# Performance work log

Measured on AMD Instinct MI355X. Metric: run time of the kernel, lower is better.

Reference implementation:

```python
import jax, jax.numpy as jnp
import numpy as np

N = 100000   # nodes
E = 1600000  # edges (avg degree 16)
D = 128      # input feature dim
H = 128      # Config.hidden_dim
G = 64       # graphs in batch
OUT = 2      # output classes


def setup_inputs() -> dict:
    key = jax.random.key(0)
    ks = jax.random.split(key, 12)
    s = 0.05
    return {
        "x": jax.random.normal(ks[0], (N, D), dtype=jnp.float32),
        "edge_index": jax.random.randint(ks[1], (2, E), 0, N),
        "batch": jnp.sort(jax.random.randint(ks[2], (N,), 0, G)),
        "W1": jax.random.normal(ks[3], (H, D), dtype=jnp.float32) * s,
        "b1": jnp.zeros((H,), jnp.float32),
        "W2": jax.random.normal(ks[4], (H, H), dtype=jnp.float32) * s,
        "b2": jnp.zeros((H,), jnp.float32),
        "Wf1": jax.random.normal(ks[5], (H, H), dtype=jnp.float32) * s,
        "bf1": jnp.zeros((H,), jnp.float32),
        "Wf2": jax.random.normal(ks[6], (OUT, H), dtype=jnp.float32) * s,
        "bf2": jnp.zeros((OUT,), jnp.float32),
    }


def _gnn_layer(x, src, dst, W, b):
    # message(x_j) = Linear(x[src]); linear commutes with gather, so transform
    # node features once (N rows) instead of per-edge (E rows): same math.
    xw = x @ W.T + b                                   # [N, H]
    msg = xw[src]                                      # [E, H] gather
    summed = jax.ops.segment_sum(msg, dst, num_segments=N)            # [N, H]
    cnt = jax.ops.segment_sum(jnp.ones((src.shape[0],), x.dtype), dst,
                              num_segments=N)                          # [N]
    return summed / jnp.maximum(cnt, 1.0)[:, None]     # scatter-mean (0 for deg-0)


def reference(x, edge_index, batch, W1, b1, W2, b2, Wf1, bf1, Wf2, bf2):
    src, dst = edge_index[0], edge_index[1]
    h = jax.nn.relu(_gnn_layer(x, src, dst, W1, b1))
    h = jax.nn.relu(_gnn_layer(h, src, dst, W2, b2))
    g = jax.ops.segment_max(h, batch, num_segments=G)  # global_max_pool [G, H]
    z = jax.nn.relu(g @ Wf1.T + bf1)                   # fc (dropout = identity, eval)
    z = z @ Wf2.T + bf2                                # [G, OUT]
    return jax.nn.log_softmax(z, axis=1)
```

## Files before the change

### kernel.cpp

```cpp
#include <hip/hip_runtime.h>
#include <hip/hip_fp16.h>
#include <math.h>


#define SPLIT 64
#define BUCKET_SHIFT 8
#define BUCKET_SIZE 256
#define MAXBUCK 512
#define BIN_CHUNK 4096
#define CAP 4608
#define LSTR 136

typedef _Float16 half8 __attribute__((ext_vector_type(8)));
typedef _Float16 half4v __attribute__((ext_vector_type(4)));
typedef _Float16 half2v __attribute__((ext_vector_type(2)));
typedef float floatx4 __attribute__((ext_vector_type(4)));
typedef float floatx2 __attribute__((ext_vector_type(2)));

#define RFL(v) __builtin_amdgcn_readfirstlane(v)

__global__ void k_init(int* __restrict__ bcur, int* __restrict__ gstart,
                       int* __restrict__ gend,
                       const float* __restrict__ W1, const float* __restrict__ W2,
                       _Float16* __restrict__ w1h, _Float16* __restrict__ w2h,
                       int G, int nbuck) {
    int i = blockIdx.x * blockDim.x + threadIdx.x;
    if (i < nbuck) bcur[i] = i * CAP;
    if (i < G) { gstart[i] = 0; gend[i] = 0; }
    w1h[i] = (_Float16)W1[i];
    w2h[i] = (_Float16)W2[i];
}

__global__ __launch_bounds__(256) void k_bin(
        const int* __restrict__ src, const int* __restrict__ dst,
        int* __restrict__ bcur, int* __restrict__ staging,
        const int* __restrict__ batch, int* __restrict__ gstart,
        int* __restrict__ gend, int E, int N, int nbuck) {
    __shared__ int lh[MAXBUCK];
    __shared__ int lbase[MAXBUCK];
    __shared__ int lc[MAXBUCK];
    int t = threadIdx.x;
    for (int i = t; i < nbuck; i += 256) { lh[i] = 0; lc[i] = 0; }

    int n = blockIdx.x * 256 + t;
    if (n < N) {
        int b = batch[n];
        if (n == 0 || batch[n - 1] != b) gstart[b] = n;
        if (n == N - 1 || batch[n + 1] != b) gend[b] = n + 1;
    }
    __syncthreads();

    int base = blockIdx.x * BIN_CHUNK;
    if (base + BIN_CHUNK <= E) {
        int ds[16], ss[16];
        const int4* dv = (const int4*)(dst + base);
        const int4* sv = (const int4*)(src + base);
        #pragma unroll
        for (int j = 0; j < 4; ++j) {
            int4 d = dv[j * 256 + t];
            int4 s = sv[j * 256 + t];
            ds[j * 4 + 0] = d.x; ds[j * 4 + 1] = d.y;
            ds[j * 4 + 2] = d.z; ds[j * 4 + 3] = d.w;
            ss[j * 4 + 0] = s.x; ss[j * 4 + 1] = s.y;
            ss[j * 4 + 2] = s.z; ss[j * 4 + 3] = s.w;
        }
        #pragma unroll
        for (int q = 0; q < 16; ++q)
            atomicAdd(&lh[ds[q] >> BUCKET_SHIFT], 1);
        __syncthreads();
        for (int i = t; i < nbuck; i += 256)
            if (lh[i]) lbase[i] = atomicAdd(&bcur[i], lh[i]);
        __syncthreads();
        #pragma unroll
        for (int q = 0; q < 16; ++q) {
            int d = ds[q];
            int b = d >> BUCKET_SHIFT;
            int pos = lbase[b] + atomicAdd(&lc[b], 1);
            if (pos < (b + 1) * CAP)
                staging[pos] = ss[q] | ((d & (BUCKET_SIZE - 1)) << 24);
        }
    } else {
        for (int e = base + t; e < E; e += 256)
            atomicAdd(&lh[dst[e] >> BUCKET_SHIFT], 1);
        __syncthreads();
        for (int i = t; i < nbuck; i += 256)
            if (lh[i]) lbase[i] = atomicAdd(&bcur[i], lh[i]);
        __syncthreads();
        for (int e = base + t; e < E; e += 256) {
            int d = dst[e];
            int b = d >> BUCKET_SHIFT;
            int pos = lbase[b] + atomicAdd(&lc[b], 1);
            if (pos < (b + 1) * CAP)
                staging[pos] = src[e] | ((d & (BUCKET_SIZE - 1)) << 24);
        }
    }
}

__global__ __launch_bounds__(BUCKET_SIZE) void k_bcsr(
        const int* __restrict__ staging, const int* __restrict__ bcur,
        int* __restrict__ esrc, int* __restrict__ rowstart,
        int* __restrict__ deg, int N) {
    __shared__ int sw[CAP];
    __shared__ int lh[BUCKET_SIZE];
    __shared__ int lcur[BUCKET_SIZE];
    __shared__ int wsum[4];
    int b = blockIdx.x;
    int s = b * CAP;
    int e = min(bcur[b], s + CAP);
    int len = e - s;
    int t = threadIdx.x;
    lh[t] = 0;
    __syncthreads();
    for (int i = t; i < len; i += BUCKET_SIZE) {
        int p = staging[s + i];
        sw[i] = p;
        atomicAdd(&lh[((unsigned)p) >> 24], 1);
    }
    __syncthreads();
    int v = lh[t];
    int lane = t & 63;
    int wv = t >> 6;
    int inc = v;
    #pragma unroll
    for (int off = 1; off < 64; off <<= 1) {
        int x = __shfl_up(inc, off, 64);
        if (lane >= off) inc += x;
    }
    if (lane == 63) wsum[wv] = inc;
    __syncthreads();
    int woff = 0;
    #pragma unroll
    for (int k = 0; k < 3; ++k)
        if (k < wv) woff += wsum[k];
    int excl = woff + inc - v;
    int node = b * BUCKET_SIZE + t;
    if (node < N) { rowstart[node] = s + excl; deg[node] = v; }
    lcur[t] = excl;
    __syncthreads();
    for (int i = t; i < len; i += BUCKET_SIZE) {
        int p = sw[i];
        int local = ((unsigned)p) >> 24;
        int pos = atomicAdd(&lcur[local], 1);
        esrc[s + pos] = p & 0xFFFFFF;
    }
}

__device__ __forceinline__ void mfma_tile(const _Float16* sX,
                                          const _Float16* __restrict__ Wh,
                                          const float* __restrict__ bias,
                                          unsigned char* __restrict__ out8,
                                          int n0, int N, int t) {
    int w = t >> 6;
    int lane = t & 63;
    int quad = lane >> 4;
    int lrow = lane & 15;

    floatx4 acc[8];
    #pragma unroll
    for (int i = 0; i < 8; ++i) acc[i] = {0.f, 0.f, 0.f, 0.f};

    int arow = (w * 16 + lrow) * LSTR + quad * 8;
    #pragma unroll
    for (int k0 = 0; k0 < 128; k0 += 32) {
        half8 a = *(const half8*)&sX[arow + k0];
        #pragma unroll
        for (int ht = 0; ht < 8; ++ht) {
            half8 b = *(const half8*)(Wh + (ht * 16 + lrow) * 128 + quad * 8 + k0);
            acc[ht] = __builtin_amdgcn_mfma_f32_16x16x32_f16(a, b, acc[ht], 0, 0, 0);
        }
    }

    #pragma unroll
    for (int ht = 0; ht < 8; ++ht) {
        int h = ht * 16 + lrow;
        float bv = bias[h];
        #pragma unroll
        for (int r = 0; r < 4; ++r) {
            int node = n0 + w * 16 + quad * 4 + r;
            if (node < N) {
                float v = acc[ht][r] + bv;
                int pk = __builtin_amdgcn_cvt_pk_fp8_f32(v, v, 0, false);
                out8[(size_t)node * 128 + h] = (unsigned char)(pk & 0xFF);
            }
        }
    }
}

__global__ __launch_bounds__(512, 6) void k_gemm(const float* __restrict__ in,
                                                 const _Float16* __restrict__ Wh,
                                                 const float* __restrict__ bias,
                                                 unsigned char* __restrict__ out8,
                                                 int N) {
    __shared__ _Float16 sX[128 * LSTR];
    int t = threadIdx.x;
    int n0 = blockIdx.x * 128;

    #pragma unroll
    for (int it = 0; it < 8; ++it) {
        int lin = it * 512 + t;
        int r = lin >> 5;
        int c = (lin & 31) * 4;
        half4v xh = {0, 0, 0, 0};
        int n = n0 + r;
        if (n < N) {
            float4 xv = *(const float4*)(in + (size_t)n * 128 + c);
            xh = half4v{ (_Float16)xv.x, (_Float16)xv.y, (_Float16)xv.z, (_Float16)xv.w };
        }
        *(half4v*)&sX[r * LSTR + c] = xh;
    }
    __syncthreads();
    mfma_tile(sX, Wh, bias, out8, n0, N, t);
}

__global__ __launch_bounds__(512, 6) void k_ag(const unsigned char* __restrict__ in8,
                                               const int* __restrict__ esrc,
                                               const int* __restrict__ rowstart,
                                               const int* __restrict__ deg,
                                               const _Float16* __restrict__ Wh,
                                               const float* __restrict__ bias,
                                               unsigned char* __restrict__ out8,
                                               int N) {
    __shared__ _Float16 sX[128 * LSTR];
    int t = threadIdx.x;
    int w = t >> 6;
    int lane = t & 63;
    int n0 = blockIdx.x * 128;
    const unsigned short* in16 = (const unsigned short*)in8;

    for (int k = 0; k < 16; ++k) {
        int node = n0 + w * 16 + k;
        float sx = 0.f, sy = 0.f;
        int dd = 0;
        if (node < N) {
            int start = RFL(rowstart[node]);
            int d     = RFL(deg[node]);
            dd = d;
            floatx2 a0 = {0.f, 0.f}, a1 = {0.f, 0.f}, a2 = {0.f, 0.f}, a3 = {0.f, 0.f};
            int i = 0;
            for (; i + 8 <= d; i += 8) {
                int x0 = RFL(esrc[start + i + 0]);
                int x1 = RFL(esrc[start + i + 1]);
                int x2 = RFL(esrc[start + i + 2]);
                int x3 = RFL(esrc[start + i + 3]);
                int x4 = RFL(esrc[start + i + 4]);
                int x5 = RFL(esrc[start + i + 5]);
                int x6 = RFL(esrc[start + i + 6]);
                int x7 = RFL(esrc[start + i + 7]);
                unsigned u0 = in16[((size_t)x0 << 6) + lane];
                unsigned u1 = in16[((size_t)x1 << 6) + lane];
                unsigned u2 = in16[((size_t)x2 << 6) + lane];
                unsigned u3 = in16[((size_t)x3 << 6) + lane];
                unsigned u4 = in16[((size_t)x4 << 6) + lane];
                unsigned u5 = in16[((size_t)x5 << 6) + lane];
                unsigned u6 = in16[((size_t)x6 << 6) + lane];
                unsigned u7 = in16[((size_t)x7 << 6) + lane];
                floatx2 f0 = __builtin_amdgcn_cvt_pk_f32_fp8(u0, false);
                floatx2 f1 = __builtin_amdgcn_cvt_pk_f32_fp8(u1, false);
                floatx2 f2 = __builtin_amdgcn_cvt_pk_f32_fp8(u2, false);
                floatx2 f3 = __builtin_amdgcn_cvt_pk_f32_fp8(u3, false);
                floatx2 f4 = __builtin_amdgcn_cvt_pk_f32_fp8(u4, false);
                floatx2 f5 = __builtin_amdgcn_cvt_pk_f32_fp8(u5, false);
                floatx2 f6 = __builtin_amdgcn_cvt_pk_f32_fp8(u6, false);
                floatx2 f7 = __builtin_amdgcn_cvt_pk_f32_fp8(u7, false);
                a0.x += f0.x; a0.y += f0.y;  a1.x += f1.x; a1.y += f1.y;
                a2.x += f2.x; a2.y += f2.y;  a3.x += f3.x; a3.y += f3.y;
                a0.x += f4.x; a0.y += f4.y;  a1.x += f5.x; a1.y += f5.y;
                a2.x += f6.x; a2.y += f6.y;  a3.x += f7.x; a3.y += f7.y;
            }
            for (; i + 4 <= d; i += 4) {
                int x0 = RFL(esrc[start + i + 0]);
                int x1 = RFL(esrc[start + i + 1]);
                int x2 = RFL(esrc[start + i + 2]);
                int x3 = RFL(esrc[start + i + 3]);
                unsigned u0 = in16[((size_t)x0 << 6) + lane];
                unsigned u1 = in16[((size_t)x1 << 6) + lane];
                unsigned u2 = in16[((size_t)x2 << 6) + lane];
                unsigned u3 = in16[((size_t)x3 << 6) + lane];
                floatx2 f0 = __builtin_amdgcn_cvt_pk_f32_fp8(u0, false);
                floatx2 f1 = __builtin_amdgcn_cvt_pk_f32_fp8(u1, false);
                floatx2 f2 = __builtin_amdgcn_cvt_pk_f32_fp8(u2, false);
                floatx2 f3 = __builtin_amdgcn_cvt_pk_f32_fp8(u3, false);
                a0.x += f0.x; a0.y += f0.y;  a1.x += f1.x; a1.y += f1.y;
                a2.x += f2.x; a2.y += f2.y;  a3.x += f3.x; a3.y += f3.y;
            }
            for (; i < d; ++i) {
                int x0 = RFL(esrc[start + i]);
                unsigned u0 = in16[((size_t)x0 << 6) + lane];
                floatx2 f0 = __builtin_amdgcn_cvt_pk_f32_fp8(u0, false);
                a0.x += f0.x; a0.y += f0.y;
            }
            sx = (a0.x + a1.x) + (a2.x + a3.x);
            sy = (a0.y + a1.y) + (a2.y + a3.y);
        }
        float dm = fmaxf((float)dd, 1.0f);
        half2v hv = { (_Float16)fmaxf(sx / dm, 0.f),
                      (_Float16)fmaxf(sy / dm, 0.f) };
        *(half2v*)&sX[(w * 16 + k) * LSTR + lane * 2] = hv;
    }
    __syncthreads();
    mfma_tile(sX, Wh, bias, out8, n0, N, t);
}

__global__ __launch_bounds__(256) void k_agg(const unsigned char* __restrict__ in8,
                                             const int* __restrict__ esrc,
                                             const int* __restrict__ rowstart,
                                             const int* __restrict__ deg,
                                             _Float16* __restrict__ outh, int N) {
    int lane = threadIdx.x & 63;
    int node = blockIdx.x * 4 + (threadIdx.x >> 6);
    if (node >= N) return;
    int start = RFL(rowstart[node]);
    int d     = RFL(deg[node]);
    const unsigned short* in16 = (const unsigned short*)in8;

    floatx2 a0 = {0.f, 0.f}, a1 = {0.f, 0.f}, a2 = {0.f, 0.f}, a3 = {0.f, 0.f};

    int i = 0;
    for (; i + 8 <= d; i += 8) {
        int x0 = RFL(esrc[start + i + 0]);
        int x1 = RFL(esrc[start + i + 1]);
        int x2 = RFL(esrc[start + i + 2]);
        int x3 = RFL(esrc[start + i + 3]);
        int x4 = RFL(esrc[start + i + 4]);
        int x5 = RFL(esrc[start + i + 5]);
        int x6 = RFL(esrc[start + i + 6]);
        int x7 = RFL(esrc[start + i + 7]);
        unsigned u0 = in16[((size_t)x0 << 6) + lane];
        unsigned u1 = in16[((size_t)x1 << 6) + lane];
        unsigned u2 = in16[((size_t)x2 << 6) + lane];
        unsigned u3 = in16[((size_t)x3 << 6) + lane];
        unsigned u4 = in16[((size_t)x4 << 6) + lane];
        unsigned u5 = in16[((size_t)x5 << 6) + lane];
        unsigned u6 = in16[((size_t)x6 << 6) + lane];
        unsigned u7 = in16[((size_t)x7 << 6) + lane];
        floatx2 f0 = __builtin_amdgcn_cvt_pk_f32_fp8(u0, false);
        floatx2 f1 = __builtin_amdgcn_cvt_pk_f32_fp8(u1, false);
        floatx2 f2 = __builtin_amdgcn_cvt_pk_f32_fp8(u2, false);
        floatx2 f3 = __builtin_amdgcn_cvt_pk_f32_fp8(u3, false);
        floatx2 f4 = __builtin_amdgcn_cvt_pk_f32_fp8(u4, false);
        floatx2 f5 = __builtin_amdgcn_cvt_pk_f32_fp8(u5, false);
        floatx2 f6 = __builtin_amdgcn_cvt_pk_f32_fp8(u6, false);
        floatx2 f7 = __builtin_amdgcn_cvt_pk_f32_fp8(u7, false);
        a0.x += f0.x; a0.y += f0.y;  a1.x += f1.x; a1.y += f1.y;
        a2.x += f2.x; a2.y += f2.y;  a3.x += f3.x; a3.y += f3.y;
        a0.x += f4.x; a0.y += f4.y;  a1.x += f5.x; a1.y += f5.y;
        a2.x += f6.x; a2.y += f6.y;  a3.x += f7.x; a3.y += f7.y;
    }
    for (; i + 4 <= d; i += 4) {
        int x0 = RFL(esrc[start + i + 0]);
        int x1 = RFL(esrc[start + i + 1]);
        int x2 = RFL(esrc[start + i + 2]);
        int x3 = RFL(esrc[start + i + 3]);
        unsigned u0 = in16[((size_t)x0 << 6) + lane];
        unsigned u1 = in16[((size_t)x1 << 6) + lane];
        unsigned u2 = in16[((size_t)x2 << 6) + lane];
        unsigned u3 = in16[((size_t)x3 << 6) + lane];
        floatx2 f0 = __builtin_amdgcn_cvt_pk_f32_fp8(u0, false);
        floatx2 f1 = __builtin_amdgcn_cvt_pk_f32_fp8(u1, false);
        floatx2 f2 = __builtin_amdgcn_cvt_pk_f32_fp8(u2, false);
        floatx2 f3 = __builtin_amdgcn_cvt_pk_f32_fp8(u3, false);
        a0.x += f0.x; a0.y += f0.y;  a1.x += f1.x; a1.y += f1.y;
        a2.x += f2.x; a2.y += f2.y;  a3.x += f3.x; a3.y += f3.y;
    }
    for (; i < d; ++i) {
        int x0 = RFL(esrc[start + i]);
        unsigned u0 = in16[((size_t)x0 << 6) + lane];
        floatx2 f0 = __builtin_amdgcn_cvt_pk_f32_fp8(u0, false);
        a0.x += f0.x; a0.y += f0.y;
    }

    float sx = (a0.x + a1.x) + (a2.x + a3.x);
    float sy = (a0.y + a1.y) + (a2.y + a3.y);
    float dm = fmaxf((float)d, 1.0f);
    half2v r = { (_Float16)fmaxf(sx / dm, 0.f),
                 (_Float16)fmaxf(sy / dm, 0.f) };
    *(half2v*)(outh + (size_t)node * 128 + lane * 2) = r;
}

__global__ void k_pool1(const _Float16* __restrict__ h, const int* __restrict__ gstart,
                        const int* __restrict__ gend, float* __restrict__ pm, int G) {
    int g = blockIdx.x / SPLIT;
    int c = blockIdx.x % SPLIT;
    int t = threadIdx.x;
    int s = gstart[g], e = gend[g];
    int len = e - s;
    int chunk = (len + SPLIT - 1) / SPLIT;
    int lo = s + c * chunk;
    int hi = min(lo + chunk, e);
    float m = -INFINITY;
    int n = lo;
    for (; n + 8 <= hi; n += 8) {
        float v0 = (float)h[(size_t)(n + 0) * 128 + t];
        float v1 = (float)h[(size_t)(n + 1) * 128 + t];
        float v2 = (float)h[(size_t)(n + 2) * 128 + t];
        float v3 = (float)h[(size_t)(n + 3) * 128 + t];
        float v4 = (float)h[(size_t)(n + 4) * 128 + t];
        float v5 = (float)h[(size_t)(n + 5) * 128 + t];
        float v6 = (float)h[(size_t)(n + 6) * 128 + t];
        float v7 = (float)h[(size_t)(n + 7) * 128 + t];
        float m0 = fmaxf(fmaxf(v0, v1), fmaxf(v2, v3));
        float m1 = fmaxf(fmaxf(v4, v5), fmaxf(v6, v7));
        m = fmaxf(m, fmaxf(m0, m1));
    }
    for (; n < hi; ++n)
        m = fmaxf(m, (float)h[(size_t)n * 128 + t]);
    pm[((size_t)g * SPLIT + c) * 128 + t] = m;
}

__global__ void k_fc(const float* __restrict__ pm,
                     const float* __restrict__ Wf1, const float* __restrict__ bf1,
                     const float* __restrict__ Wf2, const float* __restrict__ bf2,
                     float* __restrict__ out) {
    __shared__ float sg[128];
    __shared__ float sz[128];
    __shared__ float so[2];
    int g = blockIdx.x;
    int t = threadIdx.x;
    float m = -INFINITY;
    #pragma unroll 8
    for (int c = 0; c < SPLIT; ++c)
        m = fmaxf(m, pm[((size_t)g * SPLIT + c) * 128 + t]);
    sg[t] = m;
    __syncthreads();
    float z = bf1[t];
    #pragma unroll 4
    for (int d = 0; d < 128; ++d)
        z += sg[d] * Wf1[t * 128 + d];
    sz[t] = fmaxf(z, 0.f);
    __syncthreads();
    if (t < 2) {
        float o = bf2[t];
        for (int d = 0; d < 128; ++d)
            o += sz[d] * Wf2[t * 128 + d];
        so[t] = o;
    }
    __syncthreads();
    if (t == 0) {
        float a = so[0], b = so[1];
        float mx = fmaxf(a, b);
        float ls = mx + logf(expf(a - mx) + expf(b - mx));
        out[g * 2 + 0] = a - ls;
        out[g * 2 + 1] = b - ls;
    }
}

extern "C" void kernel_launch(void* const* d_in, const int* in_sizes, int n_in,
                              void* d_out, int out_size, void* d_ws, size_t ws_size,
                              hipStream_t stream) {
    const float* x   = (const float*)d_in[0];
    const int*   ei  = (const int*)d_in[1];
    const int* batch = (const int*)d_in[2];
    const float* W1  = (const float*)d_in[3];
    const float* b1  = (const float*)d_in[4];
    const float* W2  = (const float*)d_in[5];
    const float* b2  = (const float*)d_in[6];
    const float* Wf1 = (const float*)d_in[7];
    const float* bf1 = (const float*)d_in[8];
    const float* Wf2 = (const float*)d_in[9];
    const float* bf2 = (const float*)d_in[10];

    int N = in_sizes[2];
    int E = in_sizes[1] / 2;
    int G = out_size / 2;
    const int* src = ei;
    const int* dst = ei + E;
    int nbuck = (N + BUCKET_SIZE - 1) / BUCKET_SIZE;

    char* p = (char*)d_ws;
    auto alloc = [&](size_t bytes) -> char* {
        char* r = p;
        p += (bytes + 255) & ~(size_t)255;
        return r;
    };
    unsigned char* A  = (unsigned char*)alloc((size_t)N * 128);
    unsigned char* A2 = (unsigned char*)alloc((size_t)N * 128);
    _Float16* B    = (_Float16*)alloc((size_t)N * 128 * 2);
    int* deg       = (int*)alloc((size_t)N * 4);
    int* rowstart  = (int*)alloc((size_t)N * 4);
    int* esrc      = (int*)alloc((size_t)nbuck * CAP * 4);
    int* staging   = (int*)alloc((size_t)nbuck * CAP * 4);
    int* bcur      = (int*)alloc((MAXBUCK + 2) * 4);
    int* gstart    = (int*)alloc((size_t)G * 4);
    int* gend      = (int*)alloc((size_t)G * 4);
    float* pm      = (float*)alloc((size_t)G * SPLIT * 128 * 4);
    _Float16* w1h  = (_Float16*)alloc((size_t)128 * 128 * 2);
    _Float16* w2h  = (_Float16*)alloc((size_t)128 * 128 * 2);

    int nchunk = (E + BIN_CHUNK - 1) / BIN_CHUNK;

    k_init<<<64, 256, 0, stream>>>(bcur, gstart, gend, W1, W2, w1h, w2h, G, nbuck);
    k_bin<<<nchunk, 256, 0, stream>>>(src, dst, bcur, staging, batch,
                                      gstart, gend, E, N, nbuck);
    k_bcsr<<<nbuck, BUCKET_SIZE, 0, stream>>>(staging, bcur, esrc, rowstart, deg, N);

    k_gemm<<<(N + 127) / 128, 512, 0, stream>>>(x, w1h, b1, A, N);
    k_ag<<<(N + 127) / 128, 512, 0, stream>>>(A, esrc, rowstart, deg, w2h, b2, A2, N);
    k_agg<<<(N + 3) / 4, 256, 0, stream>>>(A2, esrc, rowstart, deg, B, N);
    k_pool1<<<G * SPLIT, 128, 0, stream>>>(B, gstart, gend, pm, G);
    k_fc<<<G, 128, 0, stream>>>(pm, Wf1, bf1, Wf2, bf2, (float*)d_out);
}
```

Baseline: 347.9 us.

## Split fused aggregate-GEMM and fuse global max pool into second aggregation via atomics

The fused aggregate-plus-GEMM kernel is replaced by a standalone aggregation followed by a templated GEMM that reads half-precision input. The second aggregation now pools directly into a per-graph max buffer using integer atomicMax on the non-negative post-ReLU floats. This removes the separate pool kernel, its full pass over the half-precision buffer and the SPLIT partial-max reduction. In exchange it adds an extra write and read of the intermediate buffer between the first aggregation and the second GEMM, plus atomic contention on 64×128 pool slots.

```diff
diff --git a/kernel.cpp b/kernel.cpp
--- a/kernel.cpp
+++ b/kernel.cpp
@@ -3,7 +3,6 @@
 #include <math.h>
 
 
-#define SPLIT 64
 #define BUCKET_SHIFT 8
 #define BUCKET_SIZE 256
 #define MAXBUCK 512
@@ -23,10 +22,11 @@
                        int* __restrict__ gend,
                        const float* __restrict__ W1, const float* __restrict__ W2,
                        _Float16* __restrict__ w1h, _Float16* __restrict__ w2h,
-                       int G, int nbuck) {
+                       float* __restrict__ pm, int G, int nbuck) {
     int i = blockIdx.x * blockDim.x + threadIdx.x;
     if (i < nbuck) bcur[i] = i * CAP;
     if (i < G) { gstart[i] = 0; gend[i] = 0; }
+    if (i < G * 128) pm[i] = 0.0f;
     w1h[i] = (_Float16)W1[i];
     w2h[i] = (_Float16)W2[i];
 }
@@ -145,11 +145,35 @@
     }
 }
 
-__device__ __forceinline__ void mfma_tile(const _Float16* sX,
-                                          const _Float16* __restrict__ Wh,
-                                          const float* __restrict__ bias,
-                                          unsigned char* __restrict__ out8,
-                                          int n0, int N, int t) {
+template <typename T>
+__global__ __launch_bounds__(512) void k_gemm(const T* __restrict__ in,
+                                              const _Float16* __restrict__ Wh,
+                                              const float* __restrict__ bias,
+                                              unsigned char* __restrict__ out8,
+                                              int N) {
+    __shared__ _Float16 sX[128 * LSTR];
+    int t = threadIdx.x;
+    int n0 = blockIdx.x * 128;
+
+    #pragma unroll
+    for (int it = 0; it < 8; ++it) {
+        int lin = it * 512 + t;
+        int r = lin >> 5;
+        int c = (lin & 31) * 4;
+        half4v xh = {0, 0, 0, 0};
+        int n = n0 + r;
+        if (n < N) {
+            if constexpr (sizeof(T) == 4) {
+                float4 xv = *(const float4*)((const float*)in + (size_t)n * 128 + c);
+                xh = half4v{ (_Float16)xv.x, (_Float16)xv.y, (_Float16)xv.z, (_Float16)xv.w };
+            } else {
+                xh = *(const half4v*)((const _Float16*)in + (size_t)n * 128 + c);
+            }
+        }
+        *(half4v*)&sX[r * LSTR + c] = xh;
+    }
+    __syncthreads();
+
     int w = t >> 6;
     int lane = t & 63;
     int quad = lane >> 4;
@@ -186,121 +210,6 @@
     }
 }
 
-__global__ __launch_bounds__(512, 6) void k_gemm(const float* __restrict__ in,
-                                                 const _Float16* __restrict__ Wh,
-                                                 const float* __restrict__ bias,
-                                                 unsigned char* __restrict__ out8,
-                                                 int N) {
-    __shared__ _Float16 sX[128 * LSTR];
-    int t = threadIdx.x;
-    int n0 = blockIdx.x * 128;
-
-    #pragma unroll
-    for (int it = 0; it < 8; ++it) {
-        int lin = it * 512 + t;
-        int r = lin >> 5;
-        int c = (lin & 31) * 4;
-        half4v xh = {0, 0, 0, 0};
-        int n = n0 + r;
-        if (n < N) {
-            float4 xv = *(const float4*)(in + (size_t)n * 128 + c);
-            xh = half4v{ (_Float16)xv.x, (_Float16)xv.y, (_Float16)xv.z, (_Float16)xv.w };
-        }
-        *(half4v*)&sX[r * LSTR + c] = xh;
-    }
-    __syncthreads();
-    mfma_tile(sX, Wh, bias, out8, n0, N, t);
-}
-
-__global__ __launch_bounds__(512, 6) void k_ag(const unsigned char* __restrict__ in8,
-                                               const int* __restrict__ esrc,
-                                               const int* __restrict__ rowstart,
-                                               const int* __restrict__ deg,
-                                               const _Float16* __restrict__ Wh,
-                                               const float* __restrict__ bias,
-                                               unsigned char* __restrict__ out8,
-                                               int N) {
-    __shared__ _Float16 sX[128 * LSTR];
-    int t = threadIdx.x;
-    int w = t >> 6;
-    int lane = t & 63;
-    int n0 = blockIdx.x * 128;
-    const unsigned short* in16 = (const unsigned short*)in8;
-
-    for (int k = 0; k < 16; ++k) {
-        int node = n0 + w * 16 + k;
-        float sx = 0.f, sy = 0.f;
-        int dd = 0;
-        if (node < N) {
-            int start = RFL(rowstart[node]);
-            int d     = RFL(deg[node]);
-            dd = d;
-            floatx2 a0 = {0.f, 0.f}, a1 = {0.f, 0.f}, a2 = {0.f, 0.f}, a3 = {0.f, 0.f};
-            int i = 0;
-            for (; i + 8 <= d; i += 8) {
-                int x0 = RFL(esrc[start + i + 0]);
-                int x1 = RFL(esrc[start + i + 1]);
-                int x2 = RFL(esrc[start + i + 2]);
-                int x3 = RFL(esrc[start + i + 3]);
-                int x4 = RFL(esrc[start + i + 4]);
-                int x5 = RFL(esrc[start + i + 5]);
-                int x6 = RFL(esrc[start + i + 6]);
-                int x7 = RFL(esrc[start + i + 7]);
-                unsigned u0 = in16[((size_t)x0 << 6) + lane];
-                unsigned u1 = in16[((size_t)x1 << 6) + lane];
-                unsigned u2 = in16[((size_t)x2 << 6) + lane];
-                unsigned u3 = in16[((size_t)x3 << 6) + lane];
-                unsigned u4 = in16[((size_t)x4 << 6) + lane];
-                unsigned u5 = in16[((size_t)x5 << 6) + lane];
-                unsigned u6 = in16[((size_t)x6 << 6) + lane];
-                unsigned u7 = in16[((size_t)x7 << 6) + lane];
-                floatx2 f0 = __builtin_amdgcn_cvt_pk_f32_fp8(u0, false);
-                floatx2 f1 = __builtin_amdgcn_cvt_pk_f32_fp8(u1, false);
-                floatx2 f2 = __builtin_amdgcn_cvt_pk_f32_fp8(u2, false);
-                floatx2 f3 = __builtin_amdgcn_cvt_pk_f32_fp8(u3, false);
-                floatx2 f4 = __builtin_amdgcn_cvt_pk_f32_fp8(u4, false);
-                floatx2 f5 = __builtin_amdgcn_cvt_pk_f32_fp8(u5, false);
-                floatx2 f6 = __builtin_amdgcn_cvt_pk_f32_fp8(u6, false);
-                floatx2 f7 = __builtin_amdgcn_cvt_pk_f32_fp8(u7, false);
-                a0.x += f0.x; a0.y += f0.y;  a1.x += f1.x; a1.y += f1.y;
-                a2.x += f2.x; a2.y += f2.y;  a3.x += f3.x; a3.y += f3.y;
-                a0.x += f4.x; a0.y += f4.y;  a1.x += f5.x; a1.y += f5.y;
-                a2.x += f6.x; a2.y += f6.y;  a3.x += f7.x; a3.y += f7.y;
-            }
-            for (; i + 4 <= d; i += 4) {
-                int x0 = RFL(esrc[start + i + 0]);
-                int x1 = RFL(esrc[start + i + 1]);
-                int x2 = RFL(esrc[start + i + 2]);
-                int x3 = RFL(esrc[start + i + 3]);
-                unsigned u0 = in16[((size_t)x0 << 6) + lane];
-                unsigned u1 = in16[((size_t)x1 << 6) + lane];
-                unsigned u2 = in16[((size_t)x2 << 6) + lane];
-                unsigned u3 = in16[((size_t)x3 << 6) + lane];
-                floatx2 f0 = __builtin_amdgcn_cvt_pk_f32_fp8(u0, false);
-                floatx2 f1 = __builtin_amdgcn_cvt_pk_f32_fp8(u1, false);
-                floatx2 f2 = __builtin_amdgcn_cvt_pk_f32_fp8(u2, false);
-                floatx2 f3 = __builtin_amdgcn_cvt_pk_f32_fp8(u3, false);
-                a0.x += f0.x; a0.y += f0.y;  a1.x += f1.x; a1.y += f1.y;
-                a2.x += f2.x; a2.y += f2.y;  a3.x += f3.x; a3.y += f3.y;
-            }
-            for (; i < d; ++i) {
-                int x0 = RFL(esrc[start + i]);
-                unsigned u0 = in16[((size_t)x0 << 6) + lane];
-                floatx2 f0 = __builtin_amdgcn_cvt_pk_f32_fp8(u0, false);
-                a0.x += f0.x; a0.y += f0.y;
-            }
-            sx = (a0.x + a1.x) + (a2.x + a3.x);
-            sy = (a0.y + a1.y) + (a2.y + a3.y);
-        }
-        float dm = fmaxf((float)dd, 1.0f);
-        half2v hv = { (_Float16)fmaxf(sx / dm, 0.f),
-                      (_Float16)fmaxf(sy / dm, 0.f) };
-        *(half2v*)&sX[(w * 16 + k) * LSTR + lane * 2] = hv;
-    }
-    __syncthreads();
-    mfma_tile(sX, Wh, bias, out8, n0, N, t);
-}
-
 __global__ __launch_bounds__(256) void k_agg(const unsigned char* __restrict__ in8,
                                              const int* __restrict__ esrc,
                                              const int* __restrict__ rowstart,
@@ -377,34 +286,84 @@
     *(half2v*)(outh + (size_t)node * 128 + lane * 2) = r;
 }
 
-__global__ void k_pool1(const _Float16* __restrict__ h, const int* __restrict__ gstart,
-                        const int* __restrict__ gend, float* __restrict__ pm, int G) {
-    int g = blockIdx.x / SPLIT;
-    int c = blockIdx.x % SPLIT;
-    int t = threadIdx.x;
-    int s = gstart[g], e = gend[g];
-    int len = e - s;
-    int chunk = (len + SPLIT - 1) / SPLIT;
-    int lo = s + c * chunk;
-    int hi = min(lo + chunk, e);
-    float m = -INFINITY;
-    int n = lo;
-    for (; n + 8 <= hi; n += 8) {
-        float v0 = (float)h[(size_t)(n + 0) * 128 + t];
-        float v1 = (float)h[(size_t)(n + 1) * 128 + t];
-        float v2 = (float)h[(size_t)(n + 2) * 128 + t];
-        float v3 = (float)h[(size_t)(n + 3) * 128 + t];
-        float v4 = (float)h[(size_t)(n + 4) * 128 + t];
-        float v5 = (float)h[(size_t)(n + 5) * 128 + t];
-        float v6 = (float)h[(size_t)(n + 6) * 128 + t];
-        float v7 = (float)h[(size_t)(n + 7) * 128 + t];
-        float m0 = fmaxf(fmaxf(v0, v1), fmaxf(v2, v3));
-        float m1 = fmaxf(fmaxf(v4, v5), fmaxf(v6, v7));
-        m = fmaxf(m, fmaxf(m0, m1));
-    }
-    for (; n < hi; ++n)
-        m = fmaxf(m, (float)h[(size_t)n * 128 + t]);
-    pm[((size_t)g * SPLIT + c) * 128 + t] = m;
+__global__ __launch_bounds__(256) void k_aggp(const unsigned char* __restrict__ in8,
+                                              const int* __restrict__ esrc,
+                                              const int* __restrict__ rowstart,
+                                              const int* __restrict__ deg,
+                                              const int* __restrict__ batch,
+                                              float* __restrict__ pm, int N) {
+    int lane = threadIdx.x & 63;
+    int node = blockIdx.x * 4 + (threadIdx.x >> 6);
+    if (node >= N) return;
+    int start = RFL(rowstart[node]);
+    int d     = RFL(deg[node]);
+    int g     = RFL(batch[node]);
+    const unsigned short* in16 = (const unsigned short*)in8;
+
+    floatx2 a0 = {0.f, 0.f}, a1 = {0.f, 0.f}, a2 = {0.f, 0.f}, a3 = {0.f, 0.f};
+
+    int i = 0;
+    for (; i + 8 <= d; i += 8) {
+        int x0 = RFL(esrc[start + i + 0]);
+        int x1 = RFL(esrc[start + i + 1]);
+        int x2 = RFL(esrc[start + i + 2]);
+        int x3 = RFL(esrc[start + i + 3]);
+        int x4 = RFL(esrc[start + i + 4]);
+        int x5 = RFL(esrc[start + i + 5]);
+        int x6 = RFL(esrc[start + i + 6]);
+        int x7 = RFL(esrc[start + i + 7]);
+        unsigned u0 = in16[((size_t)x0 << 6) + lane];
+        unsigned u1 = in16[((size_t)x1 << 6) + lane];
+        unsigned u2 = in16[((size_t)x2 << 6) + lane];
+        unsigned u3 = in16[((size_t)x3 << 6) + lane];
+        unsigned u4 = in16[((size_t)x4 << 6) + lane];
+        unsigned u5 = in16[((size_t)x5 << 6) + lane];
+        unsigned u6 = in16[((size_t)x6 << 6) + lane];
+        unsigned u7 = in16[((size_t)x7 << 6) + lane];
+        floatx2 f0 = __builtin_amdgcn_cvt_pk_f32_fp8(u0, false);
+        floatx2 f1 = __builtin_amdgcn_cvt_pk_f32_fp8(u1, false);
+        floatx2 f2 = __builtin_amdgcn_cvt_pk_f32_fp8(u2, false);
+        floatx2 f3 = __builtin_amdgcn_cvt_pk_f32_fp8(u3, false);
+        floatx2 f4 = __builtin_amdgcn_cvt_pk_f32_fp8(u4, false);
+        floatx2 f5 = __builtin_amdgcn_cvt_pk_f32_fp8(u5, false);
+        floatx2 f6 = __builtin_amdgcn_cvt_pk_f32_fp8(u6, false);
+        floatx2 f7 = __builtin_amdgcn_cvt_pk_f32_fp8(u7, false);
+        a0.x += f0.x; a0.y += f0.y;  a1.x += f1.x; a1.y += f1.y;
+        a2.x += f2.x; a2.y += f2.y;  a3.x += f3.x; a3.y += f3.y;
+        a0.x += f4.x; a0.y += f4.y;  a1.x += f5.x; a1.y += f5.y;
+        a2.x += f6.x; a2.y += f6.y;  a3.x += f7.x; a3.y += f7.y;
+    }
+    for (; i + 4 <= d; i += 4) {
+        int x0 = RFL(esrc[start + i + 0]);
+        int x1 = RFL(esrc[start + i + 1]);
+        int x2 = RFL(esrc[start + i + 2]);
+        int x3 = RFL(esrc[start + i + 3]);
+        unsigned u0 = in16[((size_t)x0 << 6) + lane];
+        unsigned u1 = in16[((size_t)x1 << 6) + lane];
+        unsigned u2 = in16[((size_t)x2 << 6) + lane];
+        unsigned u3 = in16[((size_t)x3 << 6) + lane];
+        floatx2 f0 = __builtin_amdgcn_cvt_pk_f32_fp8(u0, false);
+        floatx2 f1 = __builtin_amdgcn_cvt_pk_f32_fp8(u1, false);
+        floatx2 f2 = __builtin_amdgcn_cvt_pk_f32_fp8(u2, false);
+        floatx2 f3 = __builtin_amdgcn_cvt_pk_f32_fp8(u3, false);
+        a0.x += f0.x; a0.y += f0.y;  a1.x += f1.x; a1.y += f1.y;
+        a2.x += f2.x; a2.y += f2.y;  a3.x += f3.x; a3.y += f3.y;
+    }
+    for (; i < d; ++i) {
+        int x0 = RFL(esrc[start + i]);
+        unsigned u0 = in16[((size_t)x0 << 6) + lane];
+        floatx2 f0 = __builtin_amdgcn_cvt_pk_f32_fp8(u0, false);
+        a0.x += f0.x; a0.y += f0.y;
+    }
+
+    float sx = (a0.x + a1.x) + (a2.x + a3.x);
+    float sy = (a0.y + a1.y) + (a2.y + a3.y);
+    float dm = fmaxf((float)d, 1.0f);
+    float vx = fmaxf(sx / dm, 0.f);
+    float vy = fmaxf(sy / dm, 0.f);
+    int* pmi = (int*)(pm + (size_t)g * 128 + lane * 2);
+    atomicMax(pmi,     __float_as_int(vx));
+    atomicMax(pmi + 1, __float_as_int(vy));
 }
 
 __global__ void k_fc(const float* __restrict__ pm,
@@ -416,11 +375,7 @@
     __shared__ float so[2];
     int g = blockIdx.x;
     int t = threadIdx.x;
-    float m = -INFINITY;
-    #pragma unroll 8
-    for (int c = 0; c < SPLIT; ++c)
-        m = fmaxf(m, pm[((size_t)g * SPLIT + c) * 128 + t]);
-    sg[t] = m;
+    sg[t] = pm[(size_t)g * 128 + t];
     __syncthreads();
     float z = bf1[t];
     #pragma unroll 4
@@ -482,20 +437,20 @@
     int* bcur      = (int*)alloc((MAXBUCK + 2) * 4);
     int* gstart    = (int*)alloc((size_t)G * 4);
     int* gend      = (int*)alloc((size_t)G * 4);
-    float* pm      = (float*)alloc((size_t)G * SPLIT * 128 * 4);
+    float* pm      = (float*)alloc((size_t)G * 128 * 4);
     _Float16* w1h  = (_Float16*)alloc((size_t)128 * 128 * 2);
     _Float16* w2h  = (_Float16*)alloc((size_t)128 * 128 * 2);
 
     int nchunk = (E + BIN_CHUNK - 1) / BIN_CHUNK;
 
-    k_init<<<64, 256, 0, stream>>>(bcur, gstart, gend, W1, W2, w1h, w2h, G, nbuck);
+    k_init<<<64, 256, 0, stream>>>(bcur, gstart, gend, W1, W2, w1h, w2h, pm, G, nbuck);
     k_bin<<<nchunk, 256, 0, stream>>>(src, dst, bcur, staging, batch,
                                       gstart, gend, E, N, nbuck);
     k_bcsr<<<nbuck, BUCKET_SIZE, 0, stream>>>(staging, bcur, esrc, rowstart, deg, N);
 
-    k_gemm<<<(N + 127) / 128, 512, 0, stream>>>(x, w1h, b1, A, N);
-    k_ag<<<(N + 127) / 128, 512, 0, stream>>>(A, esrc, rowstart, deg, w2h, b2, A2, N);
-    k_agg<<<(N + 3) / 4, 256, 0, stream>>>(A2, esrc, rowstart, deg, B, N);
-    k_pool1<<<G * SPLIT, 128, 0, stream>>>(B, gstart, gend, pm, G);
+    k_gemm<float><<<(N + 127) / 128, 512, 0, stream>>>(x, w1h, b1, A, N);
+    k_agg<<<(N + 3) / 4, 256, 0, stream>>>(A, esrc, rowstart, deg, B, N);
+    k_gemm<_Float16><<<(N + 127) / 128, 512, 0, stream>>>(B, w2h, b2, A2, N);
+    k_aggp<<<(N + 3) / 4, 256, 0, stream>>>(A2, esrc, rowstart, deg, batch, pm, N);
     k_fc<<<G, 128, 0, stream>>>(pm, Wf1, bf1, Wf2, bf2, (float*)d_out);
 }
```

Measured after the change: 533.0 us. +53.2%, slower.
